# Kernel tuning notes

Hardware: AMD Instinct MI355X
Metric: run time of the kernel (lower is better)

The kernel has to match this reference:

```python
import jax, jax.numpy as jnp
import numpy as np

T, B, C = 2048, 4, 1024
H, K = 16, 15
PAD_L = 14  # causal: padding_l = K - 1


def setup_inputs() -> dict:
    key = jax.random.key(0)
    k1, k2 = jax.random.split(key)
    x = jax.random.normal(k1, (T, B, C), dtype=jnp.float32)
    # xavier_uniform for Linear(C, H*K): bound = sqrt(6/(fan_in+fan_out))
    bound = float(np.sqrt(6.0 / (C + H * K)))
    Wlin = jax.random.uniform(k2, (H * K, C), dtype=jnp.float32, minval=-bound, maxval=bound)
    return {"x": x, "Wlin": Wlin}


def reference(x, Wlin):
    # x: (T, B, C); Wlin: (H*K, C) -- weight_linear with no bias
    t, b, c = x.shape
    r = c // H  # channels per head
    # Generate per-position filters: (T, B, H, K)
    w = jnp.einsum('tbc,kc->tbk', x, Wlin).reshape(t, b, H, K)
    # weight_softmax=True: normalize over kernel taps
    w = jax.nn.softmax(w, axis=-1)
    # unfold1d: pad left PAD_L, right K-1-PAD_L along time, take K shifted views
    xp = jnp.pad(x, ((PAD_L, K - 1 - PAD_L), (0, 0), (0, 0)))
    # (T, B, C, K): tap k at output t reads padded position t+k
    xu = jnp.stack([xp[k:k + t] for k in range(K)], axis=-1)
    xu = xu.reshape(t, b, H, r, K)
    # batched tiny matmul: (R x K) @ (K x 1) per (t, b, h)
    out = jnp.einsum('tbhrk,tbhk->tbhr', xu, w)
    return out.reshape(t, b, c)
```

## Files before the change

### kernel.cpp

```cpp
#include <hip/hip_runtime.h>
#include <hip/hip_bf16.h>


#define T_DIM 2048
#define B_DIM 4
#define C_DIM 1024
#define H_DIM 16
#define K_TAPS 15
#define R_DIM 64
#define N_DIM (H_DIM * K_TAPS)
#define M_DIM (T_DIM * B_DIM)

typedef __attribute__((ext_vector_type(8))) short bf16x8;
typedef __attribute__((ext_vector_type(4))) float f32x4;

__device__ __forceinline__ unsigned short f2bf(float f) {
    union { float f; unsigned u; } v; v.f = f;
    return (unsigned short)((v.u + 0x7FFFu + ((v.u >> 16) & 1u)) >> 16);
}

__global__ __launch_bounds__(256) void convert_w(
    const float* __restrict__ W, unsigned short* __restrict__ Wbf)
{
    int i = (blockIdx.x * 256 + threadIdx.x) * 4;
    float4 v = *reinterpret_cast<const float4*>(W + i);
    ushort4 o;
    o.x = f2bf(v.x); o.y = f2bf(v.y); o.z = f2bf(v.z); o.w = f2bf(v.w);
    *reinterpret_cast<ushort4*>(Wbf + i) = o;
}

__global__ __launch_bounds__(64) void gemm_softmax_mfma(
    const float* __restrict__ x, const unsigned short* __restrict__ Wbf,
    float* __restrict__ wbuf)
{
    __shared__ float sm[16 * N_DIM];

    const int l   = threadIdx.x;
    const int m0  = blockIdx.x * 16;
    const int row = l & 15;
    const int kg  = l >> 4;

    f32x4 acc[15];
    #pragma unroll
    for (int nt = 0; nt < 15; ++nt) acc[nt] = (f32x4){0.f, 0.f, 0.f, 0.f};

    const float* xp = x + (size_t)(m0 + row) * C_DIM + kg * 8;
    const unsigned short* wp = Wbf + (size_t)row * C_DIM + kg * 8;

    #pragma unroll 2
    for (int ks = 0; ks < 32; ++ks) {
        const int k = ks * 32;
        float4 a0 = *reinterpret_cast<const float4*>(xp + k);
        float4 a1 = *reinterpret_cast<const float4*>(xp + k + 4);
        bf16x8 af;
        af[0] = (short)f2bf(a0.x); af[1] = (short)f2bf(a0.y);
        af[2] = (short)f2bf(a0.z); af[3] = (short)f2bf(a0.w);
        af[4] = (short)f2bf(a1.x); af[5] = (short)f2bf(a1.y);
        af[6] = (short)f2bf(a1.z); af[7] = (short)f2bf(a1.w);
        bf16x8 bfr[15];
        #pragma unroll
        for (int nt = 0; nt < 15; ++nt)
            bfr[nt] = *reinterpret_cast<const bf16x8*>(wp + (size_t)nt * 16 * C_DIM + k);
        #pragma unroll
        for (int nt = 0; nt < 15; ++nt)
            acc[nt] = __builtin_amdgcn_mfma_f32_16x16x32_bf16(af, bfr[nt], acc[nt], 0, 0, 0);
    }

    #pragma unroll
    for (int nt = 0; nt < 15; ++nt)
        #pragma unroll
        for (int j = 0; j < 4; ++j)
            sm[(kg * 4 + j) * N_DIM + nt * 16 + row] = acc[nt][j];
    __syncthreads();

    #pragma unroll
    for (int p = 0; p < 4; ++p) {
        const int idx = l * 4 + p;
        const int r = idx >> 4;
        const int h = idx & 15;
        const float* s = sm + r * N_DIM + h * K_TAPS;
        float mx = s[0];
        #pragma unroll
        for (int kk = 1; kk < K_TAPS; ++kk) mx = fmaxf(mx, s[kk]);
        float e[K_TAPS], sum = 0.f;
        #pragma unroll
        for (int kk = 0; kk < K_TAPS; ++kk) {
            e[kk] = __expf(s[kk] - mx);
            sum += e[kk];
        }
        const float inv = 1.f / sum;
        float* dst = wbuf + (size_t)(m0 + r) * N_DIM + h * K_TAPS;
        #pragma unroll
        for (int kk = 0; kk < K_TAPS; ++kk) dst[kk] = e[kk] * inv;
    }
}

__global__ __launch_bounds__(256) void conv_kernel(
    const float* __restrict__ x, const float* __restrict__ wbuf,
    float* __restrict__ out)
{
    __shared__ float xs[64 + K_TAPS - 1][R_DIM];

    const int tid = threadIdx.x;
    const int t0 = blockIdx.x * 64;
    const int bh = blockIdx.y;
    const int b = bh >> 4;
    const int h = bh & 15;
    const int cbase = h * R_DIM;

    for (int idx = tid; idx < (64 + K_TAPS - 1) * R_DIM; idx += 256) {
        int rrow = idx >> 6, r = idx & 63;
        int t = t0 - (K_TAPS - 1) + rrow;
        xs[rrow][r] = (t >= 0) ? x[((size_t)t * B_DIM + b) * C_DIM + cbase + r] : 0.f;
    }
    __syncthreads();

    const int r = tid & 63;
    const int tg = tid >> 6;
    for (int i = 0; i < 16; ++i) {
        int tl = tg * 16 + i;
        int t = t0 + tl;
        const float* wp = wbuf + ((size_t)t * B_DIM + b) * N_DIM + h * K_TAPS;
        float accv = 0.f;
        #pragma unroll
        for (int k = 0; k < K_TAPS; ++k)
            accv += wp[k] * xs[tl + k][r];
        out[((size_t)t * B_DIM + b) * C_DIM + cbase + r] = accv;
    }
}

extern "C" void kernel_launch(void* const* d_in, const int* in_sizes, int n_in,
                              void* d_out, int out_size, void* d_ws, size_t ws_size,
                              hipStream_t stream) {
    const float* x    = (const float*)d_in[0];
    const float* Wlin = (const float*)d_in[1];
    float* out  = (float*)d_out;

    float* wbuf = (float*)d_ws;
    unsigned short* Wbf = (unsigned short*)((char*)d_ws + (size_t)M_DIM * N_DIM * sizeof(float));

    convert_w<<<(N_DIM * C_DIM) / (256 * 4), 256, 0, stream>>>(Wlin, Wbf);
    gemm_softmax_mfma<<<M_DIM / 16, 64, 0, stream>>>(x, Wbf, wbuf);
    conv_kernel<<<dim3(T_DIM / 64, B_DIM * H_DIM), 256, 0, stream>>>(x, wbuf, out);
}
```

Measured before the change: 140.5 us.

## Split GEMM K-dimension across four waves and register-block the conv kernel

```diff
diff --git a/kernel.cpp b/kernel.cpp
--- a/kernel.cpp
+++ b/kernel.cpp
@@ -10,6 +10,7 @@
 #define R_DIM 64
 #define N_DIM (H_DIM * K_TAPS)
 #define M_DIM (T_DIM * B_DIM)
+#define SM_STRIDE 244
 
 typedef __attribute__((ext_vector_type(8))) short bf16x8;
 typedef __attribute__((ext_vector_type(4))) float f32x4;
@@ -29,13 +30,15 @@
     *reinterpret_cast<ushort4*>(Wbf + i) = o;
 }
 
-__global__ __launch_bounds__(64) void gemm_softmax_mfma(
+__global__ __launch_bounds__(256) void gemm_softmax_mfma(
     const float* __restrict__ x, const unsigned short* __restrict__ Wbf,
     float* __restrict__ wbuf)
 {
-    __shared__ float sm[16 * N_DIM];
+    __shared__ float sm[4][16][SM_STRIDE];
 
-    const int l   = threadIdx.x;
+    const int tid = threadIdx.x;
+    const int w   = tid >> 6;
+    const int l   = tid & 63;
     const int m0  = blockIdx.x * 16;
     const int row = l & 15;
     const int kg  = l >> 4;
@@ -44,11 +47,11 @@
     #pragma unroll
     for (int nt = 0; nt < 15; ++nt) acc[nt] = (f32x4){0.f, 0.f, 0.f, 0.f};
 
-    const float* xp = x + (size_t)(m0 + row) * C_DIM + kg * 8;
-    const unsigned short* wp = Wbf + (size_t)row * C_DIM + kg * 8;
+    const float* xp = x + (size_t)(m0 + row) * C_DIM + w * 256 + kg * 8;
+    const unsigned short* wp = Wbf + (size_t)row * C_DIM + w * 256 + kg * 8;
 
     #pragma unroll 2
-    for (int ks = 0; ks < 32; ++ks) {
+    for (int ks = 0; ks < 8; ++ks) {
         const int k = ks * 32;
         float4 a0 = *reinterpret_cast<const float4*>(xp + k);
         float4 a1 = *reinterpret_cast<const float4*>(xp + k + 4);
@@ -70,29 +73,30 @@
     for (int nt = 0; nt < 15; ++nt)
         #pragma unroll
         for (int j = 0; j < 4; ++j)
-            sm[(kg * 4 + j) * N_DIM + nt * 16 + row] = acc[nt][j];
+            sm[w][kg * 4 + j][nt * 16 + row] = acc[nt][j];
     __syncthreads();
 
+    const int r = tid >> 4;
+    const int h = tid & 15;
+    float s[K_TAPS];
     #pragma unroll
-    for (int p = 0; p < 4; ++p) {
-        const int idx = l * 4 + p;
-        const int r = idx >> 4;
-        const int h = idx & 15;
-        const float* s = sm + r * N_DIM + h * K_TAPS;
-        float mx = s[0];
-        #pragma unroll
-        for (int kk = 1; kk < K_TAPS; ++kk) mx = fmaxf(mx, s[kk]);
-        float e[K_TAPS], sum = 0.f;
-        #pragma unroll
-        for (int kk = 0; kk < K_TAPS; ++kk) {
-            e[kk] = __expf(s[kk] - mx);
-            sum += e[kk];
-        }
-        const float inv = 1.f / sum;
-        float* dst = wbuf + (size_t)(m0 + r) * N_DIM + h * K_TAPS;
-        #pragma unroll
-        for (int kk = 0; kk < K_TAPS; ++kk) dst[kk] = e[kk] * inv;
+    for (int kk = 0; kk < K_TAPS; ++kk) {
+        const int c = h * K_TAPS + kk;
+        s[kk] = sm[0][r][c] + sm[1][r][c] + sm[2][r][c] + sm[3][r][c];
     }
+    float mx = s[0];
+    #pragma unroll
+    for (int kk = 1; kk < K_TAPS; ++kk) mx = fmaxf(mx, s[kk]);
+    float sum = 0.f;
+    #pragma unroll
+    for (int kk = 0; kk < K_TAPS; ++kk) {
+        s[kk] = __expf(s[kk] - mx);
+        sum += s[kk];
+    }
+    const float inv = 1.f / sum;
+    float* dst = wbuf + (size_t)(m0 + r) * N_DIM + h * K_TAPS;
+    #pragma unroll
+    for (int kk = 0; kk < K_TAPS; ++kk) dst[kk] = s[kk] * inv;
 }
 
 __global__ __launch_bounds__(256) void conv_kernel(
@@ -108,24 +112,40 @@
     const int h = bh & 15;
     const int cbase = h * R_DIM;
 
-    for (int idx = tid; idx < (64 + K_TAPS - 1) * R_DIM; idx += 256) {
-        int rrow = idx >> 6, r = idx & 63;
+    for (int idx = tid; idx < (64 + K_TAPS - 1) * 16; idx += 256) {
+        int rrow = idx >> 4, q = idx & 15;
         int t = t0 - (K_TAPS - 1) + rrow;
-        xs[rrow][r] = (t >= 0) ? x[((size_t)t * B_DIM + b) * C_DIM + cbase + r] : 0.f;
+        float4 v = (t >= 0)
+            ? *reinterpret_cast<const float4*>(x + ((size_t)t * B_DIM + b) * C_DIM + cbase + q * 4)
+            : (float4){0.f, 0.f, 0.f, 0.f};
+        *reinterpret_cast<float4*>(&xs[rrow][q * 4]) = v;
     }
     __syncthreads();
 
     const int r = tid & 63;
-    const int tg = tid >> 6;
+    const int tg = __builtin_amdgcn_readfirstlane(tid >> 6);
+
+    float xv[31];
+    #pragma unroll
+    for (int j = 0; j < 31; ++j) xv[j] = xs[tg * 16 + j][r];
+
+    float accv[16];
+    #pragma unroll
+    for (int i = 0; i < 16; ++i) accv[i] = 0.f;
+
+    #pragma unroll
     for (int i = 0; i < 16; ++i) {
-        int tl = tg * 16 + i;
-        int t = t0 + tl;
-        const float* wp = wbuf + ((size_t)t * B_DIM + b) * N_DIM + h * K_TAPS;
-        float accv = 0.f;
+        const int t = t0 + tg * 16 + i;
+        const float* wv = wbuf + ((size_t)t * B_DIM + b) * N_DIM + h * K_TAPS;
         #pragma unroll
         for (int k = 0; k < K_TAPS; ++k)
-            accv += wp[k] * xs[tl + k][r];
-        out[((size_t)t * B_DIM + b) * C_DIM + cbase + r] = accv;
+            accv[i] += wv[k] * xv[i + k];
+    }
+
+    #pragma unroll
+    for (int i = 0; i < 16; ++i) {
+        const int t = t0 + tg * 16 + i;
+        out[((size_t)t * B_DIM + b) * C_DIM + cbase + r] = accv[i];
     }
 }
 
@@ -140,6 +160,6 @@
     unsigned short* Wbf = (unsigned short*)((char*)d_ws + (size_t)M_DIM * N_DIM * sizeof(float));
 
     convert_w<<<(N_DIM * C_DIM) / (256 * 4), 256, 0, stream>>>(Wlin, Wbf);
-    gemm_softmax_mfma<<<M_DIM / 16, 64, 0, stream>>>(x, Wbf, wbuf);
+    gemm_softmax_mfma<<<M_DIM / 16, 256, 0, stream>>>(x, Wbf, wbuf);
     conv_kernel<<<dim3(T_DIM / 64, B_DIM * H_DIM), 256, 0, stream>>>(x, wbuf, out);
 }
```

Result: faster. 127.9 us (-9.0%).
